# Kernel tuning notes

Measured on AMD Instinct MI355X. Metric: run time of the kernel, lower is better.

The kernel has to match this reference:

```python
import jax, jax.numpy as jnp
import numpy as np

L, H, D, DL, B = 32, 32, 128, 128, 512


def setup_inputs() -> dict:
    key = jax.random.key(0)
    k1, k2, k3 = jax.random.split(key, 3)
    # kaiming_normal_(mode='fan_out', nonlinearity='leaky_relu'(slope 0.01)):
    # std = gain / sqrt(fan_out), gain = sqrt(2 / (1 + 0.01^2))
    gain = np.sqrt(2.0 / (1.0 + 0.01 ** 2))
    std1 = np.float32(gain / np.sqrt(DL))  # fan_out of first Linear = latent_dim
    std2 = np.float32(gain / np.sqrt(D))   # fan_out of second Linear = input_dim
    x = jax.random.normal(k1, (B, L, H, D), dtype=jnp.float32)
    W1 = jax.random.normal(k2, (L, H, D, DL), dtype=jnp.float32) * std1  # (in, out)
    b1 = jnp.zeros((L, H, DL), dtype=jnp.float32)
    W2 = jax.random.normal(k3, (L, H, DL, D), dtype=jnp.float32) * std2
    b2 = jnp.zeros((L, H, D), dtype=jnp.float32)
    return {"x": x, "W1": W1, "b1": b1, "W2": W2, "b2": b2}


def reference(x, W1, b1, W2, b2):
    # x: [B, L, H, D]; per (l, h) position an independent Linear-GELU-Linear MLP.
    # Batched over all 1024 weight sets in two einsums (replaces the Python loop).
    h = jnp.einsum('blhd,lhde->blhe', x, W1) + b1  # [B, L, H, DL]
    h = jax.nn.gelu(h, approximate=False)          # torch nn.GELU() is exact erf
    out = jnp.einsum('blhe,lhed->blhd', h, W2) + b2  # [B, L, H, D]
    return out
```

## Files before the change

### kernel.cpp

```cpp
#include <hip/hip_runtime.h>
#include <cstdint>
#include <cstddef>

#define LH      1024
#define Dd      128
#define BT      64
#define NTILE   8
#define XSTRIDE (LH * Dd)

typedef __attribute__((ext_vector_type(8))) short bf16x8;
typedef __attribute__((ext_vector_type(4))) float f32x4;
typedef const __attribute__((address_space(1))) uint32_t gu32;
typedef __attribute__((address_space(3))) uint32_t lu32;

static __device__ __forceinline__ short f2bf(float f) {
  return __builtin_bit_cast(short, (__bf16)f);
}

static __device__ __forceinline__ float gelu_fast(float v) {
  float v2 = v * v;
  float u2 = v * (1.5957691216f + 0.0713548163f * v2);
  return v / (1.0f + __expf(-u2));
}

__global__ __launch_bounds__(256, 2) void fused_mlp_persist(
    const float* __restrict__ x, const float* __restrict__ W1,
    const float* __restrict__ b1, const float* __restrict__ W2,
    const float* __restrict__ b2, float* __restrict__ out) {
  __shared__ alignas(16) char smem[2][BT * Dd * 4];

  const int tid  = threadIdx.x;
  const int lane = tid & 63;
  const int wid  = tid >> 6;
  const int lr   = lane & 15;
  const int lg   = lane >> 4;

  const int lh = blockIdx.x;
  const int n0 = wid * 32;

  const float* w1  = W1 + (size_t)lh * (Dd * Dd);
  const float* w2  = W2 + (size_t)lh * (Dd * Dd);
  const float* xlh = x   + (size_t)lh * Dd;
  float*       olh = out + (size_t)lh * Dd;

  auto stage = [&](int t, int buf) {
#pragma unroll
    for (int i = 0; i < 8; ++i) {
      const int slot = wid * 8 + i;
      const int row  = slot * 2 + (lane >> 5);
      const int cp   = lane & 31;
      const int c    = cp ^ (row & 15);
      const float* g = xlh + (size_t)(t * BT + row) * XSTRIDE + c * 4;
      __builtin_amdgcn_global_load_lds((gu32*)g,
                                       (lu32*)(smem[buf] + slot * 1024),
                                       16, 0, 0);
    }
  };

  stage(0, 0);

  bf16x8 bw1[4][2], bw2[4][2];
#pragma unroll
  for (int ks = 0; ks < 4; ++ks)
#pragma unroll
    for (int nt = 0; nt < 2; ++nt) {
      const float* p1 = w1 + (size_t)(ks * 32 + lg * 8) * Dd + n0 + nt * 16 + lr;
      const float* p2 = w2 + (size_t)(ks * 32 + lg * 8) * Dd + n0 + nt * 16 + lr;
      bf16x8 a, b;
#pragma unroll
      for (int j = 0; j < 8; ++j) { a[j] = f2bf(p1[j * Dd]); b[j] = f2bf(p2[j * Dd]); }
      bw1[ks][nt] = a;
      bw2[ks][nt] = b;
    }

  const float bb1_0 = b1[lh * Dd + n0 + lr];
  const float bb1_1 = b1[lh * Dd + n0 + 16 + lr];
  const float bb2_0 = b2[lh * Dd + n0 + lr];
  const float bb2_1 = b2[lh * Dd + n0 + 16 + lr];

  for (int t = 0; t < NTILE; ++t) {
    const int cur = t & 1;

    __syncthreads();
    if (t + 1 < NTILE) stage(t + 1, cur ^ 1);

    f32x4 acc[4][2];
#pragma unroll
    for (int mt = 0; mt < 4; ++mt) {
      acc[mt][0] = (f32x4){bb1_0, bb1_0, bb1_0, bb1_0};
      acc[mt][1] = (f32x4){bb1_1, bb1_1, bb1_1, bb1_1};
    }
#pragma unroll
    for (int ks = 0; ks < 4; ++ks) {
      bf16x8 af[4];
#pragma unroll
      for (int mt = 0; mt < 4; ++mt) {
        const int row = mt * 16 + lr;
        const int c0  = ks * 8 + lg * 2;
        const int m   = row & 15;
        const float4 lo = *(const float4*)(smem[cur] + row * 512 + ((c0)     ^ m) * 16);
        const float4 hi = *(const float4*)(smem[cur] + row * 512 + ((c0 + 1) ^ m) * 16);
        bf16x8 a;
        a[0] = f2bf(lo.x); a[1] = f2bf(lo.y); a[2] = f2bf(lo.z); a[3] = f2bf(lo.w);
        a[4] = f2bf(hi.x); a[5] = f2bf(hi.y); a[6] = f2bf(hi.z); a[7] = f2bf(hi.w);
        af[mt] = a;
      }
#pragma unroll
      for (int mt = 0; mt < 4; ++mt)
#pragma unroll
        for (int nt = 0; nt < 2; ++nt)
          acc[mt][nt] = __builtin_amdgcn_mfma_f32_16x16x32_bf16(af[mt], bw1[ks][nt], acc[mt][nt], 0, 0, 0);
    }

    short hv[4][2][4];
#pragma unroll
    for (int mt = 0; mt < 4; ++mt)
#pragma unroll
      for (int nt = 0; nt < 2; ++nt)
#pragma unroll
        for (int r = 0; r < 4; ++r)
          hv[mt][nt][r] = f2bf(gelu_fast(acc[mt][nt][r]));

    __syncthreads();

#pragma unroll
    for (int mt = 0; mt < 4; ++mt)
#pragma unroll
      for (int nt = 0; nt < 2; ++nt) {
        const int e = n0 + nt * 16 + lr;
#pragma unroll
        for (int r = 0; r < 4; ++r) {
          const int b = mt * 16 + lg * 4 + r;
          const int off = (b * 256 + e * 2) ^ ((b & 7) << 4);
          *(short*)(smem[cur] + off) = hv[mt][nt][r];
        }
      }
    __syncthreads();

    f32x4 acc2[4][2];
#pragma unroll
    for (int mt = 0; mt < 4; ++mt) {
      acc2[mt][0] = (f32x4){bb2_0, bb2_0, bb2_0, bb2_0};
      acc2[mt][1] = (f32x4){bb2_1, bb2_1, bb2_1, bb2_1};
    }
#pragma unroll
    for (int ks = 0; ks < 4; ++ks) {
      const int k2 = (ks * 32 + lg * 8) * 2;
#pragma unroll
      for (int mt = 0; mt < 4; ++mt) {
        const int b = mt * 16 + lr;
        const int off = (b * 256 + k2) ^ ((b & 7) << 4);
        bf16x8 a = *(const bf16x8*)(smem[cur] + off);
#pragma unroll
        for (int nt = 0; nt < 2; ++nt)
          acc2[mt][nt] = __builtin_amdgcn_mfma_f32_16x16x32_bf16(a, bw2[ks][nt], acc2[mt][nt], 0, 0, 0);
      }
    }

    {
      float* ob = olh + (size_t)(t * BT) * XSTRIDE;
#pragma unroll
      for (int mt = 0; mt < 4; ++mt)
#pragma unroll
        for (int nt = 0; nt < 2; ++nt) {
          const int e = n0 + nt * 16 + lr;
#pragma unroll
          for (int r = 0; r < 4; ++r) {
            const int b = mt * 16 + lg * 4 + r;
            ob[(size_t)b * XSTRIDE + e] = acc2[mt][nt][r];
          }
        }
    }
  }
}

extern "C" void kernel_launch(void* const* d_in, const int* in_sizes, int n_in,
                              void* d_out, int out_size, void* d_ws, size_t ws_size,
                              hipStream_t stream) {
  (void)in_sizes; (void)n_in; (void)d_ws; (void)ws_size; (void)out_size;
  const float* x  = (const float*)d_in[0];
  const float* W1 = (const float*)d_in[1];
  const float* b1 = (const float*)d_in[2];
  const float* W2 = (const float*)d_in[3];
  const float* b2 = (const float*)d_in[4];
  float* out = (float*)d_out;
  fused_mlp_persist<<<dim3(LH), dim3(256), 0, stream>>>(x, W1, b1, W2, b2, out);
}
```

Before: 150.3 us.

## Use 8 waves per block with 16 columns each and defer output stores

Doubles the block to 512 threads (8 waves), so each wave owns 16 output columns instead of 32, halving per-wave register weight fragments and accumulators. It also holds each tile's second-GEMM result and writes it to global memory during the next iteration, after the next tile's prefetch is issued, so stores overlap with compute. The aim is more waves in flight to hide memory latency, at the cost of larger barrier groups and an extra register array carried across iterations.

```diff
diff --git a/kernel.cpp b/kernel.cpp
--- a/kernel.cpp
+++ b/kernel.cpp
@@ -23,7 +23,7 @@
   return v / (1.0f + __expf(-u2));
 }
 
-__global__ __launch_bounds__(256, 2) void fused_mlp_persist(
+__global__ __launch_bounds__(512, 4) void fused_mlp_persist(
     const float* __restrict__ x, const float* __restrict__ W1,
     const float* __restrict__ b1, const float* __restrict__ W2,
     const float* __restrict__ b2, float* __restrict__ out) {
@@ -36,7 +36,7 @@
   const int lg   = lane >> 4;
 
   const int lh = blockIdx.x;
-  const int n0 = wid * 32;
+  const int n0 = wid * 16;
 
   const float* w1  = W1 + (size_t)lh * (Dd * Dd);
   const float* w2  = W2 + (size_t)lh * (Dd * Dd);
@@ -45,8 +45,8 @@
 
   auto stage = [&](int t, int buf) {
 #pragma unroll
-    for (int i = 0; i < 8; ++i) {
-      const int slot = wid * 8 + i;
+    for (int i = 0; i < 4; ++i) {
+      const int slot = wid * 4 + i;
       const int row  = slot * 2 + (lane >> 5);
       const int cp   = lane & 31;
       const int c    = cp ^ (row & 15);
@@ -59,24 +59,22 @@
 
   stage(0, 0);
 
-  bf16x8 bw1[4][2], bw2[4][2];
+  bf16x8 bw1[4], bw2[4];
 #pragma unroll
-  for (int ks = 0; ks < 4; ++ks)
+  for (int ks = 0; ks < 4; ++ks) {
+    const float* p1 = w1 + (size_t)(ks * 32 + lg * 8) * Dd + n0 + lr;
+    const float* p2 = w2 + (size_t)(ks * 32 + lg * 8) * Dd + n0 + lr;
+    bf16x8 a, b;
 #pragma unroll
-    for (int nt = 0; nt < 2; ++nt) {
-      const float* p1 = w1 + (size_t)(ks * 32 + lg * 8) * Dd + n0 + nt * 16 + lr;
-      const float* p2 = w2 + (size_t)(ks * 32 + lg * 8) * Dd + n0 + nt * 16 + lr;
-      bf16x8 a, b;
-#pragma unroll
-      for (int j = 0; j < 8; ++j) { a[j] = f2bf(p1[j * Dd]); b[j] = f2bf(p2[j * Dd]); }
-      bw1[ks][nt] = a;
-      bw2[ks][nt] = b;
-    }
+    for (int j = 0; j < 8; ++j) { a[j] = f2bf(p1[j * Dd]); b[j] = f2bf(p2[j * Dd]); }
+    bw1[ks] = a;
+    bw2[ks] = b;
+  }
 
-  const float bb1_0 = b1[lh * Dd + n0 + lr];
-  const float bb1_1 = b1[lh * Dd + n0 + 16 + lr];
-  const float bb2_0 = b2[lh * Dd + n0 + lr];
-  const float bb2_1 = b2[lh * Dd + n0 + 16 + lr];
+  const float bb1 = b1[lh * Dd + n0 + lr];
+  const float bb2 = b2[lh * Dd + n0 + lr];
+
+  f32x4 accp[4];
 
   for (int t = 0; t < NTILE; ++t) {
     const int cur = t & 1;
@@ -84,12 +82,20 @@
     __syncthreads();
     if (t + 1 < NTILE) stage(t + 1, cur ^ 1);
 
-    f32x4 acc[4][2];
+    if (t > 0) {
+      float* ob = olh + (size_t)((t - 1) * BT) * XSTRIDE;
 #pragma unroll
-    for (int mt = 0; mt < 4; ++mt) {
-      acc[mt][0] = (f32x4){bb1_0, bb1_0, bb1_0, bb1_0};
-      acc[mt][1] = (f32x4){bb1_1, bb1_1, bb1_1, bb1_1};
+      for (int mt = 0; mt < 4; ++mt)
+#pragma unroll
+        for (int r = 0; r < 4; ++r) {
+          const int b = mt * 16 + lg * 4 + r;
+          ob[(size_t)b * XSTRIDE + n0 + lr] = accp[mt][r];
+        }
     }
+
+    f32x4 acc[4];
+#pragma unroll
+    for (int mt = 0; mt < 4; ++mt) acc[mt] = (f32x4){bb1, bb1, bb1, bb1};
 #pragma unroll
     for (int ks = 0; ks < 4; ++ks) {
       bf16x8 af[4];
@@ -107,42 +113,33 @@
       }
 #pragma unroll
       for (int mt = 0; mt < 4; ++mt)
-#pragma unroll
-        for (int nt = 0; nt < 2; ++nt)
-          acc[mt][nt] = __builtin_amdgcn_mfma_f32_16x16x32_bf16(af[mt], bw1[ks][nt], acc[mt][nt], 0, 0, 0);
+        acc[mt] = __builtin_amdgcn_mfma_f32_16x16x32_bf16(af[mt], bw1[ks], acc[mt], 0, 0, 0);
     }
 
-    short hv[4][2][4];
+    short hv[4][4];
 #pragma unroll
     for (int mt = 0; mt < 4; ++mt)
 #pragma unroll
-      for (int nt = 0; nt < 2; ++nt)
-#pragma unroll
-        for (int r = 0; r < 4; ++r)
-          hv[mt][nt][r] = f2bf(gelu_fast(acc[mt][nt][r]));
+      for (int r = 0; r < 4; ++r)
+        hv[mt][r] = f2bf(gelu_fast(acc[mt][r]));
 
     __syncthreads();
 
 #pragma unroll
-    for (int mt = 0; mt < 4; ++mt)
+    for (int mt = 0; mt < 4; ++mt) {
+      const int e = n0 + lr;
 #pragma unroll
-      for (int nt = 0; nt < 2; ++nt) {
-        const int e = n0 + nt * 16 + lr;
-#pragma unroll
-        for (int r = 0; r < 4; ++r) {
-          const int b = mt * 16 + lg * 4 + r;
-          const int off = (b * 256 + e * 2) ^ ((b & 7) << 4);
-          *(short*)(smem[cur] + off) = hv[mt][nt][r];
-        }
+      for (int r = 0; r < 4; ++r) {
+        const int b = mt * 16 + lg * 4 + r;
+        const int off = (b * 256 + e * 2) ^ ((b & 7) << 4);
+        *(short*)(smem[cur] + off) = hv[mt][r];
       }
+    }
     __syncthreads();
 
-    f32x4 acc2[4][2];
+    f32x4 acc2[4];
 #pragma unroll
-    for (int mt = 0; mt < 4; ++mt) {
-      acc2[mt][0] = (f32x4){bb2_0, bb2_0, bb2_0, bb2_0};
-      acc2[mt][1] = (f32x4){bb2_1, bb2_1, bb2_1, bb2_1};
-    }
+    for (int mt = 0; mt < 4; ++mt) acc2[mt] = (f32x4){bb2, bb2, bb2, bb2};
 #pragma unroll
     for (int ks = 0; ks < 4; ++ks) {
       const int k2 = (ks * 32 + lg * 8) * 2;
@@ -151,26 +148,22 @@
         const int b = mt * 16 + lr;
         const int off = (b * 256 + k2) ^ ((b & 7) << 4);
         bf16x8 a = *(const bf16x8*)(smem[cur] + off);
-#pragma unroll
-        for (int nt = 0; nt < 2; ++nt)
-          acc2[mt][nt] = __builtin_amdgcn_mfma_f32_16x16x32_bf16(a, bw2[ks][nt], acc2[mt][nt], 0, 0, 0);
+        acc2[mt] = __builtin_amdgcn_mfma_f32_16x16x32_bf16(a, bw2[ks], acc2[mt], 0, 0, 0);
       }
     }
+#pragma unroll
+    for (int mt = 0; mt < 4; ++mt) accp[mt] = acc2[mt];
+  }
 
-    {
-      float* ob = olh + (size_t)(t * BT) * XSTRIDE;
+  {
+    float* ob = olh + (size_t)((NTILE - 1) * BT) * XSTRIDE;
 #pragma unroll
-      for (int mt = 0; mt < 4; ++mt)
+    for (int mt = 0; mt < 4; ++mt)
 #pragma unroll
-        for (int nt = 0; nt < 2; ++nt) {
-          const int e = n0 + nt * 16 + lr;
-#pragma unroll
-          for (int r = 0; r < 4; ++r) {
-            const int b = mt * 16 + lg * 4 + r;
-            ob[(size_t)b * XSTRIDE + e] = acc2[mt][nt][r];
-          }
-        }
-    }
+      for (int r = 0; r < 4; ++r) {
+        const int b = mt * 16 + lg * 4 + r;
+        ob[(size_t)b * XSTRIDE + n0 + lr] = accp[mt][r];
+      }
   }
 }
 
@@ -184,5 +177,5 @@
   const float* W2 = (const float*)d_in[3];
   const float* b2 = (const float*)d_in[4];
   float* out = (float*)d_out;
-  fused_mlp_persist<<<dim3(LH), dim3(256), 0, stream>>>(x, W1, b1, W2, b2, out);
+  fused_mlp_persist<<<dim3(LH), dim3(512), 0, stream>>>(x, W1, b1, W2, b2, out);
 }
```

New measurement: 191.1 us. 27.1% more time.

## Load x directly into registers, split batch across two blocks per weight set

Applied to the files above, without the earlier changes.

Replaces the LDS staging of x tiles through global_load_lds with direct per-lane float4 register loads, software-prefetched one k-step ahead. The batch is split in half so each (l,h) weight set gets two blocks (2048 total) with a remapped block index, and occupancy is raised to 3 blocks per CU with LDS shrunk to a double-buffered bf16 hidden tile. One barrier per tile is removed by double-buffering the hidden activations. Weights are now loaded and converted twice per weight set, and the register prefetch adds register pressure.

```diff
diff --git a/kernel.cpp b/kernel.cpp
--- a/kernel.cpp
+++ b/kernel.cpp
@@ -5,13 +5,11 @@
 #define LH      1024
 #define Dd      128
 #define BT      64
-#define NTILE   8
+#define NTILE   4
 #define XSTRIDE (LH * Dd)
 
 typedef __attribute__((ext_vector_type(8))) short bf16x8;
 typedef __attribute__((ext_vector_type(4))) float f32x4;
-typedef const __attribute__((address_space(1))) uint32_t gu32;
-typedef __attribute__((address_space(3))) uint32_t lu32;
 
 static __device__ __forceinline__ short f2bf(float f) {
   return __builtin_bit_cast(short, (__bf16)f);
@@ -23,11 +21,18 @@
   return v / (1.0f + __expf(-u2));
 }
 
-__global__ __launch_bounds__(256, 2) void fused_mlp_persist(
+#define BAR_LGKM() do {                                          \
+  __builtin_amdgcn_sched_barrier(0);                             \
+  asm volatile("s_waitcnt lgkmcnt(0)" ::: "memory");             \
+  __builtin_amdgcn_s_barrier();                                  \
+  __builtin_amdgcn_sched_barrier(0);                             \
+} while (0)
+
+__global__ __launch_bounds__(256, 3) void fused_mlp_direct(
     const float* __restrict__ x, const float* __restrict__ W1,
     const float* __restrict__ b1, const float* __restrict__ W2,
     const float* __restrict__ b2, float* __restrict__ out) {
-  __shared__ alignas(16) char smem[2][BT * Dd * 4];
+  __shared__ alignas(16) short Hs[2][BT * Dd];
 
   const int tid  = threadIdx.x;
   const int lane = tid & 63;
@@ -35,29 +40,24 @@
   const int lr   = lane & 15;
   const int lg   = lane >> 4;
 
-  const int lh = blockIdx.x;
-  const int n0 = wid * 32;
+  const int bid = blockIdx.x;
+  const int lh   = (bid & 7) * 128 + (bid >> 4);
+  const int half = (bid >> 3) & 1;
+  const int row0 = half * (NTILE * BT);
+  const int n0   = wid * 32;
 
-  const float* w1  = W1 + (size_t)lh * (Dd * Dd);
-  const float* w2  = W2 + (size_t)lh * (Dd * Dd);
-  const float* xlh = x   + (size_t)lh * Dd;
-  float*       olh = out + (size_t)lh * Dd;
+  const float* w1 = W1 + (size_t)lh * (Dd * Dd);
+  const float* w2 = W2 + (size_t)lh * (Dd * Dd);
+  const float* xa = x + ((size_t)(row0 + lr) * LH + lh) * Dd + lg * 8;
+  float* oa = out + ((size_t)row0 * LH + lh) * Dd;
 
-  auto stage = [&](int t, int buf) {
+  float4 xf[4][2];
 #pragma unroll
-    for (int i = 0; i < 8; ++i) {
-      const int slot = wid * 8 + i;
-      const int row  = slot * 2 + (lane >> 5);
-      const int cp   = lane & 31;
-      const int c    = cp ^ (row & 15);
-      const float* g = xlh + (size_t)(t * BT + row) * XSTRIDE + c * 4;
-      __builtin_amdgcn_global_load_lds((gu32*)g,
-                                       (lu32*)(smem[buf] + slot * 1024),
-                                       16, 0, 0);
-    }
-  };
-
-  stage(0, 0);
+  for (int mt = 0; mt < 4; ++mt) {
+    const float4* p = (const float4*)(xa + (size_t)(mt * 16) * XSTRIDE);
+    xf[mt][0] = p[0];
+    xf[mt][1] = p[1];
+  }
 
   bf16x8 bw1[4][2], bw2[4][2];
 #pragma unroll
@@ -79,10 +79,7 @@
   const float bb2_1 = b2[lh * Dd + n0 + 16 + lr];
 
   for (int t = 0; t < NTILE; ++t) {
-    const int cur = t & 1;
-
-    __syncthreads();
-    if (t + 1 < NTILE) stage(t + 1, cur ^ 1);
+    const int c = t & 1;
 
     f32x4 acc[4][2];
 #pragma unroll
@@ -90,26 +87,27 @@
       acc[mt][0] = (f32x4){bb1_0, bb1_0, bb1_0, bb1_0};
       acc[mt][1] = (f32x4){bb1_1, bb1_1, bb1_1, bb1_1};
     }
+
 #pragma unroll
     for (int ks = 0; ks < 4; ++ks) {
-      bf16x8 af[4];
 #pragma unroll
       for (int mt = 0; mt < 4; ++mt) {
-        const int row = mt * 16 + lr;
-        const int c0  = ks * 8 + lg * 2;
-        const int m   = row & 15;
-        const float4 lo = *(const float4*)(smem[cur] + row * 512 + ((c0)     ^ m) * 16);
-        const float4 hi = *(const float4*)(smem[cur] + row * 512 + ((c0 + 1) ^ m) * 16);
+        const float4 lo = xf[mt][0], hi = xf[mt][1];
+        if (ks < 3) {
+          const float4* p = (const float4*)(xa + (size_t)(t * BT + mt * 16) * XSTRIDE + (ks + 1) * 32);
+          xf[mt][0] = p[0];
+          xf[mt][1] = p[1];
+        } else if (t + 1 < NTILE) {
+          const float4* p = (const float4*)(xa + (size_t)((t + 1) * BT + mt * 16) * XSTRIDE);
+          xf[mt][0] = p[0];
+          xf[mt][1] = p[1];
+        }
         bf16x8 a;
         a[0] = f2bf(lo.x); a[1] = f2bf(lo.y); a[2] = f2bf(lo.z); a[3] = f2bf(lo.w);
         a[4] = f2bf(hi.x); a[5] = f2bf(hi.y); a[6] = f2bf(hi.z); a[7] = f2bf(hi.w);
-        af[mt] = a;
+        acc[mt][0] = __builtin_amdgcn_mfma_f32_16x16x32_bf16(a, bw1[ks][0], acc[mt][0], 0, 0, 0);
+        acc[mt][1] = __builtin_amdgcn_mfma_f32_16x16x32_bf16(a, bw1[ks][1], acc[mt][1], 0, 0, 0);
       }
-#pragma unroll
-      for (int mt = 0; mt < 4; ++mt)
-#pragma unroll
-        for (int nt = 0; nt < 2; ++nt)
-          acc[mt][nt] = __builtin_amdgcn_mfma_f32_16x16x32_bf16(af[mt], bw1[ks][nt], acc[mt][nt], 0, 0, 0);
     }
 
     short hv[4][2][4];
@@ -121,8 +119,6 @@
         for (int r = 0; r < 4; ++r)
           hv[mt][nt][r] = f2bf(gelu_fast(acc[mt][nt][r]));
 
-    __syncthreads();
-
 #pragma unroll
     for (int mt = 0; mt < 4; ++mt)
 #pragma unroll
@@ -132,10 +128,11 @@
         for (int r = 0; r < 4; ++r) {
           const int b = mt * 16 + lg * 4 + r;
           const int off = (b * 256 + e * 2) ^ ((b & 7) << 4);
-          *(short*)(smem[cur] + off) = hv[mt][nt][r];
+          *(short*)((char*)Hs[c] + off) = hv[mt][nt][r];
         }
       }
-    __syncthreads();
+
+    BAR_LGKM();
 
     f32x4 acc2[4][2];
 #pragma unroll
@@ -150,7 +147,7 @@
       for (int mt = 0; mt < 4; ++mt) {
         const int b = mt * 16 + lr;
         const int off = (b * 256 + k2) ^ ((b & 7) << 4);
-        bf16x8 a = *(const bf16x8*)(smem[cur] + off);
+        bf16x8 a = *(const bf16x8*)((const char*)Hs[c] + off);
 #pragma unroll
         for (int nt = 0; nt < 2; ++nt)
           acc2[mt][nt] = __builtin_amdgcn_mfma_f32_16x16x32_bf16(a, bw2[ks][nt], acc2[mt][nt], 0, 0, 0);
@@ -158,7 +155,7 @@
     }
 
     {
-      float* ob = olh + (size_t)(t * BT) * XSTRIDE;
+      float* ob = oa + (size_t)(t * BT) * XSTRIDE;
 #pragma unroll
       for (int mt = 0; mt < 4; ++mt)
 #pragma unroll
@@ -184,5 +181,5 @@
   const float* W2 = (const float*)d_in[3];
   const float* b2 = (const float*)d_in[4];
   float* out = (float*)d_out;
-  fused_mlp_persist<<<dim3(LH), dim3(256), 0, stream>>>(x, W1, b1, W2, b2, out);
+  fused_mlp_direct<<<dim3(2048), dim3(256), 0, stream>>>(x, W1, b1, W2, b2, out);
 }
```

Result: slower. 432.6 us (+187.8%).
